# Kernel optimization log

Measured on AMD Instinct MI355X. Metric: run time of the kernel, lower is better.

The kernel has to match this reference:

```python
import jax, jax.numpy as jnp
import numpy as np

H = 8  # num_heads

def setup_inputs() -> dict:
    key = jax.random.key(0)
    ks = jax.random.split(key, 10)
    B, N, C = 2048, 50, 256
    x = jax.random.normal(ks[0], (B, N, C), dtype=jnp.float32)
    adj = jax.random.uniform(ks[1], (B, N, N), dtype=jnp.float32)
    matrix = jax.random.normal(ks[2], (B, N, N), dtype=jnp.float32)
    s = 0.02
    Wq = jax.random.normal(ks[3], (C, C), dtype=jnp.float32) * s
    bq = jnp.zeros((C,), dtype=jnp.float32)
    Wk = jax.random.normal(ks[4], (C, C), dtype=jnp.float32) * s
    bk = jnp.zeros((C,), dtype=jnp.float32)
    Wa = jax.random.normal(ks[5], (N * H, N), dtype=jnp.float32) * s
    ba = jnp.zeros((N * H,), dtype=jnp.float32)
    Wm = jax.random.normal(ks[6], (N * H, N), dtype=jnp.float32) * s
    bm = jnp.zeros((N * H,), dtype=jnp.float32)
    lambdas = jnp.tile(jnp.array([[1.0, 0.0, 0.0]], dtype=jnp.float32), (H, 1))
    return {"x": x, "adj": adj, "matrix": matrix, "Wq": Wq, "bq": bq,
            "Wk": Wk, "bk": bk, "Wa": Wa, "ba": ba, "Wm": Wm, "bm": bm,
            "lambdas": lambdas}

def reference(x, adj, matrix, Wq, bq, Wk, bk, Wa, ba, Wm, bm, lambdas):
    B, N, C = x.shape
    D = C // H
    # torch Linear: y = x @ W.T + b
    q = (jnp.einsum('bnc,dc->bnd', x, Wq) + bq).reshape(B, N, H, D).transpose(0, 2, 1, 3)
    k = (jnp.einsum('bnc,dc->bnd', x, Wk) + bk).reshape(B, N, H, D).transpose(0, 2, 1, 3)
    # NOTE: original code computes v with self.k (faithful to source)
    v = k
    # scale uses full dim C (x.shape[-1]), not head_dim, as in source
    attn = jax.nn.softmax(jnp.einsum('bhnd,bhmd->bhnm', q, k) * (C ** -0.5), axis=-1)
    adj_a = jax.nn.softmax(
        (jnp.einsum('bnm,km->bnk', adj, Wa) + ba).reshape(B, N, H, N).transpose(0, 2, 1, 3), axis=-1)
    mat_a = jax.nn.softmax(
        (jnp.einsum('bnm,km->bnk', matrix, Wm) + bm).reshape(B, N, H, N).transpose(0, 2, 1, 3), axis=-1)
    lam = jax.nn.softmax(lambdas, axis=-1)  # [H, 3]
    l0 = lam[:, 0][None, :, None, None]
    l1 = lam[:, 1][None, :, None, None]
    l2 = lam[:, 2][None, :, None, None]
    mix = l0 * attn + l1 * adj_a + l2 * mat_a  # [B, H, N, N]
    out = jnp.einsum('bhnm,bhmd->bhnd', mix, v).transpose(0, 2, 1, 3).reshape(B, N, C)
    return out
```

## Files before the change

### kernel.cpp

```cpp
#include <hip/hip_runtime.h>
#include <stdint.h>


typedef __attribute__((ext_vector_type(8))) short short8;
typedef __attribute__((ext_vector_type(4))) float f32x4;
typedef unsigned short u16;

#define L2E 1.4426950408889634f

__device__ __forceinline__ u16 f2bf(float f) {
  unsigned int u = __float_as_uint(f);
  u = (u + 0x7FFFu + ((u >> 16) & 1u)) >> 16;
  return (u16)u;
}
__device__ __forceinline__ unsigned cvt_pk_bf16(float a, float b) {
  unsigned r;
  asm("v_cvt_pk_bf16_f32 %0, %1, %2" : "=v"(r) : "v"(a), "v"(b));
  return r;
}
__device__ __forceinline__ float exp2_fast(float x) {
#if __has_builtin(__builtin_amdgcn_exp2f)
  return __builtin_amdgcn_exp2f(x);
#else
  return __expf(x * 0.6931471805599453f);
#endif
}
__device__ __forceinline__ void lds_fence() {
  asm volatile("s_waitcnt lgkmcnt(0)");
}

__global__ __launch_bounds__(256) void cast_all(
    const float* __restrict__ adj, const float* __restrict__ mat,
    const float* __restrict__ Wq, const float* __restrict__ Wk,
    const float* __restrict__ Wa, const float* __restrict__ Wm,
    const float* __restrict__ ba, const float* __restrict__ bm,
    u16* __restrict__ da, u16* __restrict__ dm, u16* __restrict__ wqk,
    u16* __restrict__ wab, u16* __restrict__ wmb,
    float* __restrict__ bap, float* __restrict__ bmp, float* __restrict__ maskv,
    u16* __restrict__ qws, u16* __restrict__ kws) {
  const int blk = blockIdx.x, tid = threadIdx.x;
  if (blk < 2048) {
    const int total8 = (102416 * 64) / 8;
    for (int i8 = blk * 256 + tid; i8 < total8; i8 += 2048 * 256) {
      int r = i8 >> 3, c = (i8 & 7) * 8;
      short8 oa = (short8){0,0,0,0,0,0,0,0};
      short8 om = (short8){0,0,0,0,0,0,0,0};
      if (r < 102400) {
        size_t base = (size_t)r * 50;
#pragma unroll
        for (int p = 0; p < 4; ++p) {
          int col = c + 2 * p;
          if (col < 50) {
            float2 va = *(const float2*)(adj + base + col);
            float2 vm = *(const float2*)(mat + base + col);
            oa[2*p] = f2bf(va.x); oa[2*p+1] = f2bf(va.y);
            om[2*p] = f2bf(vm.x); om[2*p+1] = f2bf(vm.y);
          }
        }
      }
      *(short8*)(da + (size_t)i8 * 8) = oa;
      *(short8*)(dm + (size_t)i8 * 8) = om;
    }
  } else if (blk < 2112) {
    int idx8 = (blk - 2048) * 256 + tid;
    int r = idx8 >> 5, c = (idx8 & 31) * 8;
    const float* src = (r < 256) ? (Wq + (size_t)r * 256 + c)
                                 : (Wk + (size_t)(r - 256) * 256 + c);
    float4 v0 = *(const float4*)(src);
    float4 v1 = *(const float4*)(src + 4);
    short8 o;
    o[0] = f2bf(v0.x); o[1] = f2bf(v0.y); o[2] = f2bf(v0.z); o[3] = f2bf(v0.w);
    o[4] = f2bf(v1.x); o[5] = f2bf(v1.y); o[6] = f2bf(v1.z); o[7] = f2bf(v1.w);
    *(short8*)(wqk + (size_t)idx8 * 8) = o;
  } else if (blk < 2216) {
    int idx = (blk - 2112) * 256 + tid;
    int r = idx >> 6, c = idx & 63;
    float va = 0.f, vm = 0.f;
    if (r < 400 && c < 50) { va = Wa[r * 50 + c]; vm = Wm[r * 50 + c]; }
    wab[idx] = f2bf(va); wmb[idx] = f2bf(vm);
  } else {
    short8 z = (short8){0,0,0,0,0,0,0,0};
    *(short8*)(qws + (size_t)819200 * 32 + tid * 8) = z;
    *(short8*)(kws + (size_t)819200 * 32 + tid * 8) = z;
#pragma unroll
    for (int j = 0; j < 2; ++j) {
      int idx = tid + 256 * j;
      int hh = idx >> 6, m = idx & 63;
      bap[idx] = (m < 50) ? ba[hh * 50 + m] * L2E : -1.0e30f;
      bmp[idx] = (m < 50) ? bm[hh * 50 + m] * L2E : -1.0e30f;
    }
    if (tid < 64) maskv[tid] = (tid < 50) ? 0.f : -1.0e30f;
  }
}

__global__ __launch_bounds__(256) void proj_kernel(
    const float* __restrict__ x, const u16* __restrict__ wqk,
    const float* __restrict__ bq, const float* __restrict__ bk,
    u16* __restrict__ qws, u16* __restrict__ kws) {
  __shared__ char xa[64 * 512];
  __shared__ char wb[64 * 512];
  const int tid = threadIdx.x;
  const int m0 = blockIdx.x * 64;

#pragma unroll
  for (int t = 0; t < 16; ++t) {
    int idx = tid + t * 256;
    int r = idx >> 6, c4 = idx & 63;
    float4 v = *(const float4*)(x + (size_t)(m0 + r) * 256 + c4 * 4);
    unsigned long long pk = (unsigned long long)f2bf(v.x)
                          | ((unsigned long long)f2bf(v.y) << 16)
                          | ((unsigned long long)f2bf(v.z) << 32)
                          | ((unsigned long long)f2bf(v.w) << 48);
    int byte = (r * 512 + c4 * 8) ^ ((r & 7) << 4);
    *(unsigned long long*)(xa + byte) = pk;
  }
  __syncthreads();

  const int w = tid >> 6, l = tid & 63, lo = l & 15, g = l >> 4;
  short8 a[8];
  const int ra = 16 * w + lo;
#pragma unroll
  for (int ks = 0; ks < 8; ++ks)
    a[ks] = *(const short8*)(xa + ((ra * 512 + ks * 64 + g * 16) ^ ((ra & 7) << 4)));
  size_t mb[4];
#pragma unroll
  for (int i = 0; i < 4; ++i) {
    int m = m0 + 16 * w + 4 * g + i;
    int b = m / 50;
    int n = m - 50 * b;
    mb[i] = (size_t)b * 12800 + (size_t)n * 32;
  }

  for (int nt = 0; nt < 8; ++nt) {
    __syncthreads();
#pragma unroll
    for (int t = 0; t < 8; ++t) {
      int idx = tid + t * 256;
      int r = idx >> 5, c8 = idx & 31;
      short8 v = *(const short8*)(wqk + (size_t)(nt * 64 + r) * 256 + c8 * 8);
      int byte = (r * 512 + c8 * 16) ^ ((r & 7) << 4);
      *(short8*)(wb + byte) = v;
    }
    __syncthreads();

    f32x4 acc[4];
#pragma unroll
    for (int tj = 0; tj < 4; ++tj) acc[tj] = (f32x4){0.f, 0.f, 0.f, 0.f};
#pragma unroll
    for (int ks = 0; ks < 8; ++ks) {
#pragma unroll
      for (int tj = 0; tj < 4; ++tj) {
        int rb = 16 * tj + lo;
        short8 bb = *(const short8*)(wb + ((rb * 512 + ks * 64 + g * 16) ^ ((rb & 7) << 4)));
        acc[tj] = __builtin_amdgcn_mfma_f32_16x16x32_bf16(a[ks], bb, acc[tj], 0, 0, 0);
      }
    }
    const int n0 = nt * 64;
#pragma unroll
    for (int tj = 0; tj < 4; ++tj) {
      int j = n0 + 16 * tj + lo;
      int jj = j & 255;
      float bias = (j < 256) ? bq[jj] : bk[jj];
      u16* dst = (j < 256) ? qws : kws;
      int hh = jj >> 5, d = jj & 31;
#pragma unroll
      for (int i = 0; i < 4; ++i)
        dst[mb[i] + (size_t)hh * 1600 + d] = f2bf(acc[tj][i] + bias);
    }
  }
}


__device__ __forceinline__ void sm_pv_tile(
    f32x4 (&S)[4], const f32x4 (&bml)[4], float sl2e, float lam,
    u16* pb, const short8 (&vb)[2][2], f32x4 (&Otj)[2], int buf, int lo, int g) {
  float p[4][4];
#pragma unroll
  for (int ti = 0; ti < 4; ++ti)
#pragma unroll
    for (int i = 0; i < 4; ++i)
      p[ti][i] = exp2_fast(S[ti][i] * sl2e + bml[ti][i]);
  float t0 = (p[0][0] + p[0][1]) + (p[0][2] + p[0][3]);
  float t1 = (p[1][0] + p[1][1]) + (p[1][2] + p[1][3]);
  float t2 = (p[2][0] + p[2][1]) + (p[2][2] + p[2][3]);
  float t3 = (p[3][0] + p[3][1]) + (p[3][2] + p[3][3]);
  float sum = (t0 + t1) + (t2 + t3);
  sum += __shfl_xor(sum, 16);
  sum += __shfl_xor(sum, 32);
  float r = lam * __builtin_amdgcn_rcpf(sum);
  u16* base = pb + buf * 1152 + lo * 72;
#pragma unroll
  for (int ti = 0; ti < 4; ++ti) {
    uint2 pk;
    pk.x = cvt_pk_bf16(p[ti][0] * r, p[ti][1] * r);
    pk.y = cvt_pk_bf16(p[ti][2] * r, p[ti][3] * r);
    *(uint2*)(base + 16 * ti + 4 * g) = pk;
  }
  lds_fence();
#pragma unroll
  for (int ks = 0; ks < 2; ++ks) {
    short8 pa = *(const short8*)(pb + buf * 1152 + lo * 72 + ks * 32 + g * 8);
#pragma unroll
    for (int tjv = 0; tjv < 2; ++tjv)
      Otj[tjv] = __builtin_amdgcn_mfma_f32_16x16x32_bf16(pa, vb[tjv][ks], Otj[tjv], 0, 0, 0);
  }
}

__device__ __forceinline__ void adj_phase(
    const u16* __restrict__ aBase, const u16* __restrict__ bBase,
    const float* __restrict__ bPad, float lam,
    u16* pb, const short8 (&vb)[2][2], f32x4 (&O)[2][2], int half, int lo, int g) {
  short8 af[4][2];
#pragma unroll
  for (int ti = 0; ti < 4; ++ti)
#pragma unroll
    for (int ks = 0; ks < 2; ++ks)
      af[ti][ks] = *(const short8*)(aBase + (size_t)(lo + 16 * ti) * 64 + ks * 32 + g * 8);
  short8 bf[2][2];
#pragma unroll
  for (int tjl = 0; tjl < 2; ++tjl) {
    int n = lo + 16 * (2 * half + tjl);
#pragma unroll
    for (int ks = 0; ks < 2; ++ks)
      bf[tjl][ks] = *(const short8*)(bBase + (size_t)n * 64 + ks * 32 + g * 8);
  }
  f32x4 bml[4];
#pragma unroll
  for (int ti = 0; ti < 4; ++ti)
    bml[ti] = *(const f32x4*)(bPad + 16 * ti + 4 * g);
#pragma unroll
  for (int tjl = 0; tjl < 2; ++tjl) {
    f32x4 S[4];
#pragma unroll
    for (int ti = 0; ti < 4; ++ti) S[ti] = (f32x4){0.f, 0.f, 0.f, 0.f};
#pragma unroll
    for (int ti = 0; ti < 4; ++ti)
      S[ti] = __builtin_amdgcn_mfma_f32_16x16x32_bf16(af[ti][0], bf[tjl][0], S[ti], 0, 0, 0);
#pragma unroll
    for (int ti = 0; ti < 4; ++ti)
      S[ti] = __builtin_amdgcn_mfma_f32_16x16x32_bf16(af[ti][1], bf[tjl][1], S[ti], 0, 0, 0);
    sm_pv_tile(S, bml, L2E, lam, pb, vb, O[tjl], tjl, lo, g);
  }
}

__global__ __launch_bounds__(256) void attn_kernel(
    const u16* __restrict__ qws, const u16* __restrict__ kws,
    const u16* __restrict__ adjb, const u16* __restrict__ matb,
    const u16* __restrict__ wab, const u16* __restrict__ wmb,
    const float* __restrict__ bap, const float* __restrict__ bmp,
    const float* __restrict__ maskv,
    const float* __restrict__ lambdas, float* __restrict__ out) {
  __shared__ u16 smem[4][2304];
  const int tid = threadIdx.x;
  const int w = tid >> 6, l = tid & 63, lo = l & 15, g = l >> 4;
  const int bh = blockIdx.x * 2 + (w >> 1);
  const int half = w & 1;
  const int b = bh >> 3, h = bh & 7;
  u16* sh = smem[w];

  float la = lambdas[h * 3 + 0], lb = lambdas[h * 3 + 1], lc = lambdas[h * 3 + 2];
  float lmx = fmaxf(la, fmaxf(lb, lc));
  float e0 = __expf(la - lmx), e1 = __expf(lb - lmx), e2 = __expf(lc - lmx);
  float einv = 1.f / (e0 + e1 + e2);
  float lam0 = e0 * einv, lam1 = e1 * einv, lam2 = e2 * einv;

  {
    const u16* kr = kws + (size_t)bh * 1600 + (size_t)l * 32;
#pragma unroll
    for (int ch = 0; ch < 4; ++ch) {
      short8 v = (short8){0, 0, 0, 0, 0, 0, 0, 0};
      if (l < 50) v = *(const short8*)(kr + ch * 8);
#pragma unroll
      for (int jj = 0; jj < 8; ++jj)
        sh[(ch * 8 + jj) * 72 + l] = (u16)v[jj];
    }
  }
  lds_fence();
  short8 vb[2][2];
#pragma unroll
  for (int tjv = 0; tjv < 2; ++tjv)
#pragma unroll
    for (int ks = 0; ks < 2; ++ks)
      vb[tjv][ks] = *(const short8*)(sh + (lo + 16 * tjv) * 72 + ks * 32 + g * 8);

  f32x4 O[2][2];
#pragma unroll
  for (int tjl = 0; tjl < 2; ++tjl)
#pragma unroll
    for (int tjv = 0; tjv < 2; ++tjv) O[tjl][tjv] = (f32x4){0.f, 0.f, 0.f, 0.f};

  {
    short8 af[4];
#pragma unroll
    for (int ti = 0; ti < 4; ++ti)
      af[ti] = *(const short8*)(kws + (size_t)bh * 1600 + (size_t)(lo + 16 * ti) * 32 + g * 8);
    short8 qf[2];
#pragma unroll
    for (int tjl = 0; tjl < 2; ++tjl)
      qf[tjl] = *(const short8*)(qws + (size_t)bh * 1600 +
                                 (size_t)(lo + 16 * (2 * half + tjl)) * 32 + g * 8);
    f32x4 bml[4];
#pragma unroll
    for (int ti = 0; ti < 4; ++ti)
      bml[ti] = *(const f32x4*)(maskv + 16 * ti + 4 * g);
#pragma unroll
    for (int tjl = 0; tjl < 2; ++tjl) {
      f32x4 S[4];
#pragma unroll
      for (int ti = 0; ti < 4; ++ti) S[ti] = (f32x4){0.f, 0.f, 0.f, 0.f};
#pragma unroll
      for (int ti = 0; ti < 4; ++ti)
        S[ti] = __builtin_amdgcn_mfma_f32_16x16x32_bf16(af[ti], qf[tjl], S[ti], 0, 0, 0);
      sm_pv_tile(S, bml, 0.0625f * L2E, lam0, sh, vb, O[tjl], tjl, lo, g);
    }
  }
  adj_phase(wab + (size_t)h * 3200, adjb + (size_t)b * 3200, bap + h * 64,
            lam1, sh, vb, O, half, lo, g);
  adj_phase(wmb + (size_t)h * 3200, matb + (size_t)b * 3200, bmp + h * 64,
            lam2, sh, vb, O, half, lo, g);

  float* ob = out + (size_t)b * 12800 + h * 32;
#pragma unroll
  for (int tjl = 0; tjl < 2; ++tjl) {
    int tj = 2 * half + tjl;
#pragma unroll
    for (int i = 0; i < 4; ++i) {
      int n = 16 * tj + 4 * g + i;
      if (n < 50) {
#pragma unroll
        for (int tjv = 0; tjv < 2; ++tjv)
          ob[(size_t)n * 256 + 16 * tjv + lo] = O[tjl][tjv][i];
      }
    }
  }
}

extern "C" void kernel_launch(void* const* d_in, const int* in_sizes, int n_in,
                              void* d_out, int out_size, void* d_ws, size_t ws_size,
                              hipStream_t stream) {
  const float* x       = (const float*)d_in[0];
  const float* adj     = (const float*)d_in[1];
  const float* mat     = (const float*)d_in[2];
  const float* Wq      = (const float*)d_in[3];
  const float* bq      = (const float*)d_in[4];
  const float* Wk      = (const float*)d_in[5];
  const float* bk      = (const float*)d_in[6];
  const float* Wa      = (const float*)d_in[7];
  const float* ba      = (const float*)d_in[8];
  const float* Wm      = (const float*)d_in[9];
  const float* bm      = (const float*)d_in[10];
  const float* lambdas = (const float*)d_in[11];
  float* out = (float*)d_out;

  char* ws = (char*)d_ws;
  u16* wqk    = (u16*)ws; ws += (size_t)512 * 256 * 2;
  u16* wab    = (u16*)ws; ws += (size_t)416 * 64 * 2;
  u16* wmb    = (u16*)ws; ws += (size_t)416 * 64 * 2;
  float* bap  = (float*)ws; ws += (size_t)512 * 4;
  float* bmp  = (float*)ws; ws += (size_t)512 * 4;
  float* mskv = (float*)ws; ws += (size_t)64 * 4;
  u16* adjb   = (u16*)ws; ws += (size_t)102416 * 64 * 2;
  u16* matb   = (u16*)ws; ws += (size_t)102416 * 64 * 2;
  u16* qws    = (u16*)ws; ws += (size_t)819264 * 32 * 2;
  u16* kws    = (u16*)ws; ws += (size_t)819264 * 32 * 2;

  cast_all<<<2217, 256, 0, stream>>>(adj, mat, Wq, Wk, Wa, Wm, ba, bm,
                                     adjb, matb, wqk, wab, wmb,
                                     bap, bmp, mskv, qws, kws);
  proj_kernel<<<1600, 256, 0, stream>>>(x, wqk, bq, bk, qws, kws);
  attn_kernel<<<8192, 256, 0, stream>>>(qws, kws, adjb, matb, wab, wmb,
                                        bap, bmp, mskv, lambdas, out);
}
```

Baseline: 233.6 us.

## Process two batches per wave across all query tiles to interleave independent work

Each wave now computes the full 50x50 attention for one head across two batch elements, where before a pair of waves split the query tiles of a single batch-head. The two independent streams are interleaved so the MFMA, exp and LDS round-trips of one can hide the latency of the other, and the Wa/Wm weight fragments are loaded once and reused for both batches. The explicit lgkmcnt fences are replaced by volatile LDS accesses, the grid shrinks to a quarter of its former size, and launch bounds request 2 blocks per CU. Risks are much higher register pressure from the doubled accumulators and fragments, and fewer waves available to hide latency.

Measured after the change: 234.5 us. Within noise of the previous version (+0.4%).

```diff
diff --git a/kernel.cpp b/kernel.cpp
--- a/kernel.cpp
+++ b/kernel.cpp
@@ -4,6 +4,8 @@
 
 typedef __attribute__((ext_vector_type(8))) short short8;
 typedef __attribute__((ext_vector_type(4))) float f32x4;
+typedef __attribute__((ext_vector_type(2))) unsigned u32x2;
+typedef __attribute__((ext_vector_type(4))) unsigned u32x4;
 typedef unsigned short u16;
 
 #define L2E 1.4426950408889634f
@@ -24,9 +26,6 @@
 #else
   return __expf(x * 0.6931471805599453f);
 #endif
-}
-__device__ __forceinline__ void lds_fence() {
-  asm volatile("s_waitcnt lgkmcnt(0)");
 }
 
 __global__ __launch_bounds__(256) void cast_all(
@@ -171,9 +170,9 @@
 }
 
 
-__device__ __forceinline__ void sm_pv_tile(
+__device__ __forceinline__ void sm_store(
     f32x4 (&S)[4], const f32x4 (&bml)[4], float sl2e, float lam,
-    u16* pb, const short8 (&vb)[2][2], f32x4 (&Otj)[2], int buf, int lo, int g) {
+    u16* pb, int buf, int lo, int g) {
   float p[4][4];
 #pragma unroll
   for (int ti = 0; ti < 4; ++ti)
@@ -188,75 +187,45 @@
   sum += __shfl_xor(sum, 16);
   sum += __shfl_xor(sum, 32);
   float r = lam * __builtin_amdgcn_rcpf(sum);
-  u16* base = pb + buf * 1152 + lo * 72;
 #pragma unroll
   for (int ti = 0; ti < 4; ++ti) {
-    uint2 pk;
+    u32x2 pk;
     pk.x = cvt_pk_bf16(p[ti][0] * r, p[ti][1] * r);
     pk.y = cvt_pk_bf16(p[ti][2] * r, p[ti][3] * r);
-    *(uint2*)(base + 16 * ti + 4 * g) = pk;
-  }
-  lds_fence();
+    *(volatile u32x2*)(pb + buf * 1152 + lo * 72 + 16 * ti + 4 * g) = pk;
+  }
+}
+
+__device__ __forceinline__ void pv_acc(
+    const u16* pb, int buf, const short8 (&vbS)[2][2], f32x4 (&Otj)[2],
+    int lo, int g) {
 #pragma unroll
   for (int ks = 0; ks < 2; ++ks) {
-    short8 pa = *(const short8*)(pb + buf * 1152 + lo * 72 + ks * 32 + g * 8);
+    u32x4 t = *(const volatile u32x4*)(pb + buf * 1152 + lo * 72 + ks * 32 + g * 8);
+    short8 pa = __builtin_bit_cast(short8, t);
 #pragma unroll
     for (int tjv = 0; tjv < 2; ++tjv)
-      Otj[tjv] = __builtin_amdgcn_mfma_f32_16x16x32_bf16(pa, vb[tjv][ks], Otj[tjv], 0, 0, 0);
-  }
-}
-
-__device__ __forceinline__ void adj_phase(
-    const u16* __restrict__ aBase, const u16* __restrict__ bBase,
-    const float* __restrict__ bPad, float lam,
-    u16* pb, const short8 (&vb)[2][2], f32x4 (&O)[2][2], int half, int lo, int g) {
-  short8 af[4][2];
-#pragma unroll
-  for (int ti = 0; ti < 4; ++ti)
-#pragma unroll
-    for (int ks = 0; ks < 2; ++ks)
-      af[ti][ks] = *(const short8*)(aBase + (size_t)(lo + 16 * ti) * 64 + ks * 32 + g * 8);
-  short8 bf[2][2];
-#pragma unroll
-  for (int tjl = 0; tjl < 2; ++tjl) {
-    int n = lo + 16 * (2 * half + tjl);
-#pragma unroll
-    for (int ks = 0; ks < 2; ++ks)
-      bf[tjl][ks] = *(const short8*)(bBase + (size_t)n * 64 + ks * 32 + g * 8);
-  }
-  f32x4 bml[4];
-#pragma unroll
-  for (int ti = 0; ti < 4; ++ti)
-    bml[ti] = *(const f32x4*)(bPad + 16 * ti + 4 * g);
-#pragma unroll
-  for (int tjl = 0; tjl < 2; ++tjl) {
-    f32x4 S[4];
-#pragma unroll
-    for (int ti = 0; ti < 4; ++ti) S[ti] = (f32x4){0.f, 0.f, 0.f, 0.f};
-#pragma unroll
-    for (int ti = 0; ti < 4; ++ti)
-      S[ti] = __builtin_amdgcn_mfma_f32_16x16x32_bf16(af[ti][0], bf[tjl][0], S[ti], 0, 0, 0);
-#pragma unroll
-    for (int ti = 0; ti < 4; ++ti)
-      S[ti] = __builtin_amdgcn_mfma_f32_16x16x32_bf16(af[ti][1], bf[tjl][1], S[ti], 0, 0, 0);
-    sm_pv_tile(S, bml, L2E, lam, pb, vb, O[tjl], tjl, lo, g);
-  }
-}
-
-__global__ __launch_bounds__(256) void attn_kernel(
+      Otj[tjv] = __builtin_amdgcn_mfma_f32_16x16x32_bf16(pa, vbS[tjv][ks], Otj[tjv], 0, 0, 0);
+  }
+}
+
+__global__ __launch_bounds__(256, 2) void attn_kernel(
     const u16* __restrict__ qws, const u16* __restrict__ kws,
     const u16* __restrict__ adjb, const u16* __restrict__ matb,
     const u16* __restrict__ wab, const u16* __restrict__ wmb,
     const float* __restrict__ bap, const float* __restrict__ bmp,
     const float* __restrict__ maskv,
     const float* __restrict__ lambdas, float* __restrict__ out) {
-  __shared__ u16 smem[4][2304];
+  __shared__ u16 smem[4][2][2304];
   const int tid = threadIdx.x;
   const int w = tid >> 6, l = tid & 63, lo = l & 15, g = l >> 4;
-  const int bh = blockIdx.x * 2 + (w >> 1);
-  const int half = w & 1;
-  const int b = bh >> 3, h = bh & 7;
-  u16* sh = smem[w];
+  const int wid = blockIdx.x * 4 + w;
+  const int h = wid & 7;
+  const int bp = wid >> 3;
+  const int b0 = 2 * bp, b1 = 2 * bp + 1;
+  const int bh0 = b0 * 8 + h, bh1 = b1 * 8 + h;
+  u16* pb0 = smem[w][0];
+  u16* pb1 = smem[w][1];
 
   float la = lambdas[h * 3 + 0], lb = lambdas[h * 3 + 1], lc = lambdas[h * 3 + 2];
   float lmx = fmaxf(la, fmaxf(lb, lc));
@@ -265,73 +234,132 @@
   float lam0 = e0 * einv, lam1 = e1 * einv, lam2 = e2 * einv;
 
   {
-    const u16* kr = kws + (size_t)bh * 1600 + (size_t)l * 32;
+    const u16* kr0 = kws + (size_t)bh0 * 1600 + (size_t)l * 32;
+    const u16* kr1 = kws + (size_t)bh1 * 1600 + (size_t)l * 32;
 #pragma unroll
     for (int ch = 0; ch < 4; ++ch) {
-      short8 v = (short8){0, 0, 0, 0, 0, 0, 0, 0};
-      if (l < 50) v = *(const short8*)(kr + ch * 8);
-#pragma unroll
-      for (int jj = 0; jj < 8; ++jj)
-        sh[(ch * 8 + jj) * 72 + l] = (u16)v[jj];
-    }
-  }
-  lds_fence();
-  short8 vb[2][2];
+      short8 v0 = (short8){0,0,0,0,0,0,0,0};
+      short8 v1 = (short8){0,0,0,0,0,0,0,0};
+      if (l < 50) {
+        v0 = *(const short8*)(kr0 + ch * 8);
+        v1 = *(const short8*)(kr1 + ch * 8);
+      }
+#pragma unroll
+      for (int jj = 0; jj < 8; ++jj) {
+        *(volatile u16*)(pb0 + (ch * 8 + jj) * 72 + l) = (u16)v0[jj];
+        *(volatile u16*)(pb1 + (ch * 8 + jj) * 72 + l) = (u16)v1[jj];
+      }
+    }
+  }
+  short8 vb0[2][2], vb1[2][2];
 #pragma unroll
   for (int tjv = 0; tjv < 2; ++tjv)
 #pragma unroll
-    for (int ks = 0; ks < 2; ++ks)
-      vb[tjv][ks] = *(const short8*)(sh + (lo + 16 * tjv) * 72 + ks * 32 + g * 8);
-
-  f32x4 O[2][2];
-#pragma unroll
-  for (int tjl = 0; tjl < 2; ++tjl)
-#pragma unroll
-    for (int tjv = 0; tjv < 2; ++tjv) O[tjl][tjv] = (f32x4){0.f, 0.f, 0.f, 0.f};
+    for (int ks = 0; ks < 2; ++ks) {
+      u32x4 t0 = *(const volatile u32x4*)(pb0 + (lo + 16 * tjv) * 72 + ks * 32 + g * 8);
+      u32x4 t1 = *(const volatile u32x4*)(pb1 + (lo + 16 * tjv) * 72 + ks * 32 + g * 8);
+      vb0[tjv][ks] = __builtin_bit_cast(short8, t0);
+      vb1[tjv][ks] = __builtin_bit_cast(short8, t1);
+    }
+
+  f32x4 O[2][4][2];
+#pragma unroll
+  for (int s = 0; s < 2; ++s)
+#pragma unroll
+    for (int tj = 0; tj < 4; ++tj)
+#pragma unroll
+      for (int tjv = 0; tjv < 2; ++tjv) O[s][tj][tjv] = (f32x4){0.f,0.f,0.f,0.f};
 
   {
-    short8 af[4];
-#pragma unroll
-    for (int ti = 0; ti < 4; ++ti)
-      af[ti] = *(const short8*)(kws + (size_t)bh * 1600 + (size_t)(lo + 16 * ti) * 32 + g * 8);
-    short8 qf[2];
-#pragma unroll
-    for (int tjl = 0; tjl < 2; ++tjl)
-      qf[tjl] = *(const short8*)(qws + (size_t)bh * 1600 +
-                                 (size_t)(lo + 16 * (2 * half + tjl)) * 32 + g * 8);
+    short8 af0[4], af1[4];
+#pragma unroll
+    for (int ti = 0; ti < 4; ++ti) {
+      af0[ti] = *(const short8*)(kws + (size_t)bh0 * 1600 + (size_t)(lo + 16 * ti) * 32 + g * 8);
+      af1[ti] = *(const short8*)(kws + (size_t)bh1 * 1600 + (size_t)(lo + 16 * ti) * 32 + g * 8);
+    }
     f32x4 bml[4];
 #pragma unroll
     for (int ti = 0; ti < 4; ++ti)
       bml[ti] = *(const f32x4*)(maskv + 16 * ti + 4 * g);
 #pragma unroll
-    for (int tjl = 0; tjl < 2; ++tjl) {
-      f32x4 S[4];
-#pragma unroll
-      for (int ti = 0; ti < 4; ++ti) S[ti] = (f32x4){0.f, 0.f, 0.f, 0.f};
-#pragma unroll
-      for (int ti = 0; ti < 4; ++ti)
-        S[ti] = __builtin_amdgcn_mfma_f32_16x16x32_bf16(af[ti], qf[tjl], S[ti], 0, 0, 0);
-      sm_pv_tile(S, bml, 0.0625f * L2E, lam0, sh, vb, O[tjl], tjl, lo, g);
-    }
-  }
-  adj_phase(wab + (size_t)h * 3200, adjb + (size_t)b * 3200, bap + h * 64,
-            lam1, sh, vb, O, half, lo, g);
-  adj_phase(wmb + (size_t)h * 3200, matb + (size_t)b * 3200, bmp + h * 64,
-            lam2, sh, vb, O, half, lo, g);
-
-  float* ob = out + (size_t)b * 12800 + h * 32;
-#pragma unroll
-  for (int tjl = 0; tjl < 2; ++tjl) {
-    int tj = 2 * half + tjl;
-#pragma unroll
-    for (int i = 0; i < 4; ++i) {
-      int n = 16 * tj + 4 * g + i;
-      if (n < 50) {
-#pragma unroll
-        for (int tjv = 0; tjv < 2; ++tjv)
-          ob[(size_t)n * 256 + 16 * tjv + lo] = O[tjl][tjv][i];
-      }
-    }
+    for (int tj = 0; tj < 4; ++tj) {
+      short8 qf0 = *(const short8*)(qws + (size_t)bh0 * 1600 + (size_t)(lo + 16 * tj) * 32 + g * 8);
+      short8 qf1 = *(const short8*)(qws + (size_t)bh1 * 1600 + (size_t)(lo + 16 * tj) * 32 + g * 8);
+      f32x4 S0[4], S1[4];
+#pragma unroll
+      for (int ti = 0; ti < 4; ++ti) { S0[ti] = (f32x4){0,0,0,0}; S1[ti] = (f32x4){0,0,0,0}; }
+#pragma unroll
+      for (int ti = 0; ti < 4; ++ti) {
+        S0[ti] = __builtin_amdgcn_mfma_f32_16x16x32_bf16(af0[ti], qf0, S0[ti], 0, 0, 0);
+        S1[ti] = __builtin_amdgcn_mfma_f32_16x16x32_bf16(af1[ti], qf1, S1[ti], 0, 0, 0);
+      }
+      sm_store(S0, bml, 0.0625f * L2E, lam0, pb0, tj & 1, lo, g);
+      sm_store(S1, bml, 0.0625f * L2E, lam0, pb1, tj & 1, lo, g);
+      pv_acc(pb0, tj & 1, vb0, O[0][tj], lo, g);
+      pv_acc(pb1, tj & 1, vb1, O[1][tj], lo, g);
+    }
+  }
+#pragma unroll
+  for (int ph = 0; ph < 2; ++ph) {
+    const u16* aBase = (ph == 0 ? wab : wmb) + (size_t)h * 3200;
+    const u16* bB0 = (ph == 0 ? adjb : matb) + (size_t)b0 * 3200;
+    const u16* bB1 = (ph == 0 ? adjb : matb) + (size_t)b1 * 3200;
+    const float* bPad = (ph == 0 ? bap : bmp) + h * 64;
+    float lamp = (ph == 0) ? lam1 : lam2;
+
+    short8 afw[4][2];
+#pragma unroll
+    for (int ti = 0; ti < 4; ++ti)
+#pragma unroll
+      for (int ks = 0; ks < 2; ++ks)
+        afw[ti][ks] = *(const short8*)(aBase + (size_t)(lo + 16 * ti) * 64 + ks * 32 + g * 8);
+    f32x4 bml[4];
+#pragma unroll
+    for (int ti = 0; ti < 4; ++ti)
+      bml[ti] = *(const f32x4*)(bPad + 16 * ti + 4 * g);
+
+#pragma unroll
+    for (int tj = 0; tj < 4; ++tj) {
+      short8 bf0[2], bf1[2];
+#pragma unroll
+      for (int ks = 0; ks < 2; ++ks) {
+        bf0[ks] = *(const short8*)(bB0 + (size_t)(lo + 16 * tj) * 64 + ks * 32 + g * 8);
+        bf1[ks] = *(const short8*)(bB1 + (size_t)(lo + 16 * tj) * 64 + ks * 32 + g * 8);
+      }
+      f32x4 S0[4], S1[4];
+#pragma unroll
+      for (int ti = 0; ti < 4; ++ti) { S0[ti] = (f32x4){0,0,0,0}; S1[ti] = (f32x4){0,0,0,0}; }
+#pragma unroll
+      for (int ti = 0; ti < 4; ++ti) {
+        S0[ti] = __builtin_amdgcn_mfma_f32_16x16x32_bf16(afw[ti][0], bf0[0], S0[ti], 0, 0, 0);
+        S1[ti] = __builtin_amdgcn_mfma_f32_16x16x32_bf16(afw[ti][0], bf1[0], S1[ti], 0, 0, 0);
+      }
+#pragma unroll
+      for (int ti = 0; ti < 4; ++ti) {
+        S0[ti] = __builtin_amdgcn_mfma_f32_16x16x32_bf16(afw[ti][1], bf0[1], S0[ti], 0, 0, 0);
+        S1[ti] = __builtin_amdgcn_mfma_f32_16x16x32_bf16(afw[ti][1], bf1[1], S1[ti], 0, 0, 0);
+      }
+      sm_store(S0, bml, L2E, lamp, pb0, tj & 1, lo, g);
+      sm_store(S1, bml, L2E, lamp, pb1, tj & 1, lo, g);
+      pv_acc(pb0, tj & 1, vb0, O[0][tj], lo, g);
+      pv_acc(pb1, tj & 1, vb1, O[1][tj], lo, g);
+    }
+  }
+
+#pragma unroll
+  for (int s = 0; s < 2; ++s) {
+    float* ob = out + (size_t)(s ? b1 : b0) * 12800 + h * 32;
+#pragma unroll
+    for (int tj = 0; tj < 4; ++tj)
+#pragma unroll
+      for (int i = 0; i < 4; ++i) {
+        int n = 16 * tj + 4 * g + i;
+        if (n < 50) {
+#pragma unroll
+          for (int tjv = 0; tjv < 2; ++tjv)
+            ob[(size_t)n * 256 + 16 * tjv + lo] = O[s][tj][tjv][i];
+        }
+      }
   }
 }
 
@@ -368,6 +396,6 @@
                                      adjb, matb, wqk, wab, wmb,
                                      bap, bmp, mskv, qws, kws);
   proj_kernel<<<1600, 256, 0, stream>>>(x, wqk, bq, bk, qws, kws);
-  attn_kernel<<<8192, 256, 0, stream>>>(qws, kws, adjb, matb, wab, wmb,
+  attn_kernel<<<2048, 256, 0, stream>>>(qws, kws, adjb, matb, wab, wmb,
                                         bap, bmp, mskv, lambdas, out);
 }
```

## Assign one wave per batch-head and hoist global loads ahead of compute

Applied to the files above, without the earlier changes.

Each wave now processes all four query tiles of a batch-head instead of splitting them across two waves, halving the grid. This removes redundant K transposes, K/weight fragment loads and adj/mat loads per head. Global loads for K, Q, adj and mat are issued early with scheduling barriers to overlap latency, and the explicit LDS wait is replaced with volatile LDS accesses. It raises register pressure and drops zeroing of padded K rows.

Measured after the change: 232.4 us. No clear change (-0.5%).

```diff
diff --git a/kernel.cpp b/kernel.cpp
--- a/kernel.cpp
+++ b/kernel.cpp
@@ -4,6 +4,8 @@
 
 typedef __attribute__((ext_vector_type(8))) short short8;
 typedef __attribute__((ext_vector_type(4))) float f32x4;
+typedef __attribute__((ext_vector_type(2))) unsigned u32x2;
+typedef __attribute__((ext_vector_type(4))) unsigned u32x4;
 typedef unsigned short u16;
 
 #define L2E 1.4426950408889634f
@@ -24,9 +26,6 @@
 #else
   return __expf(x * 0.6931471805599453f);
 #endif
-}
-__device__ __forceinline__ void lds_fence() {
-  asm volatile("s_waitcnt lgkmcnt(0)");
 }
 
 __global__ __launch_bounds__(256) void cast_all(
@@ -170,10 +169,9 @@
   }
 }
 
-
-__device__ __forceinline__ void sm_pv_tile(
+__device__ __forceinline__ void sm_store(
     f32x4 (&S)[4], const f32x4 (&bml)[4], float sl2e, float lam,
-    u16* pb, const short8 (&vb)[2][2], f32x4 (&Otj)[2], int buf, int lo, int g) {
+    u16* pb, int buf, int lo, int g) {
   float p[4][4];
 #pragma unroll
   for (int ti = 0; ti < 4; ++ti)
@@ -188,58 +186,25 @@
   sum += __shfl_xor(sum, 16);
   sum += __shfl_xor(sum, 32);
   float r = lam * __builtin_amdgcn_rcpf(sum);
-  u16* base = pb + buf * 1152 + lo * 72;
 #pragma unroll
   for (int ti = 0; ti < 4; ++ti) {
-    uint2 pk;
+    u32x2 pk;
     pk.x = cvt_pk_bf16(p[ti][0] * r, p[ti][1] * r);
     pk.y = cvt_pk_bf16(p[ti][2] * r, p[ti][3] * r);
-    *(uint2*)(base + 16 * ti + 4 * g) = pk;
-  }
-  lds_fence();
+    *(volatile u32x2*)(pb + buf * 1152 + lo * 72 + 16 * ti + 4 * g) = pk;
+  }
+}
+
+__device__ __forceinline__ void pv_acc(
+    const u16* pb, int buf, const short8 (&vbS)[2][2], f32x4 (&Otj)[2],
+    int lo, int g) {
 #pragma unroll
   for (int ks = 0; ks < 2; ++ks) {
-    short8 pa = *(const short8*)(pb + buf * 1152 + lo * 72 + ks * 32 + g * 8);
+    u32x4 t = *(const volatile u32x4*)(pb + buf * 1152 + lo * 72 + ks * 32 + g * 8);
+    short8 pa = __builtin_bit_cast(short8, t);
 #pragma unroll
     for (int tjv = 0; tjv < 2; ++tjv)
-      Otj[tjv] = __builtin_amdgcn_mfma_f32_16x16x32_bf16(pa, vb[tjv][ks], Otj[tjv], 0, 0, 0);
-  }
-}
-
-__device__ __forceinline__ void adj_phase(
-    const u16* __restrict__ aBase, const u16* __restrict__ bBase,
-    const float* __restrict__ bPad, float lam,
-    u16* pb, const short8 (&vb)[2][2], f32x4 (&O)[2][2], int half, int lo, int g) {
-  short8 af[4][2];
-#pragma unroll
-  for (int ti = 0; ti < 4; ++ti)
-#pragma unroll
-    for (int ks = 0; ks < 2; ++ks)
-      af[ti][ks] = *(const short8*)(aBase + (size_t)(lo + 16 * ti) * 64 + ks * 32 + g * 8);
-  short8 bf[2][2];
-#pragma unroll
-  for (int tjl = 0; tjl < 2; ++tjl) {
-    int n = lo + 16 * (2 * half + tjl);
-#pragma unroll
-    for (int ks = 0; ks < 2; ++ks)
-      bf[tjl][ks] = *(const short8*)(bBase + (size_t)n * 64 + ks * 32 + g * 8);
-  }
-  f32x4 bml[4];
-#pragma unroll
-  for (int ti = 0; ti < 4; ++ti)
-    bml[ti] = *(const f32x4*)(bPad + 16 * ti + 4 * g);
-#pragma unroll
-  for (int tjl = 0; tjl < 2; ++tjl) {
-    f32x4 S[4];
-#pragma unroll
-    for (int ti = 0; ti < 4; ++ti) S[ti] = (f32x4){0.f, 0.f, 0.f, 0.f};
-#pragma unroll
-    for (int ti = 0; ti < 4; ++ti)
-      S[ti] = __builtin_amdgcn_mfma_f32_16x16x32_bf16(af[ti][0], bf[tjl][0], S[ti], 0, 0, 0);
-#pragma unroll
-    for (int ti = 0; ti < 4; ++ti)
-      S[ti] = __builtin_amdgcn_mfma_f32_16x16x32_bf16(af[ti][1], bf[tjl][1], S[ti], 0, 0, 0);
-    sm_pv_tile(S, bml, L2E, lam, pb, vb, O[tjl], tjl, lo, g);
+      Otj[tjv] = __builtin_amdgcn_mfma_f32_16x16x32_bf16(pa, vbS[tjv][ks], Otj[tjv], 0, 0, 0);
   }
 }
 
@@ -253,10 +218,32 @@
   __shared__ u16 smem[4][2304];
   const int tid = threadIdx.x;
   const int w = tid >> 6, l = tid & 63, lo = l & 15, g = l >> 4;
-  const int bh = blockIdx.x * 2 + (w >> 1);
-  const int half = w & 1;
+  const int bh = blockIdx.x * 4 + w;
   const int b = bh >> 3, h = bh & 7;
   u16* sh = smem[w];
+
+  const u16* kbase = kws + (size_t)bh * 1600;
+  const u16* qbase = qws + (size_t)bh * 1600;
+
+  short8 kr[4];
+#pragma unroll
+  for (int ch = 0; ch < 4; ++ch)
+    kr[ch] = *(const short8*)(kbase + (size_t)l * 32 + ch * 8);
+  short8 af1[4], qf1[4];
+#pragma unroll
+  for (int ti = 0; ti < 4; ++ti)
+    af1[ti] = *(const short8*)(kbase + (size_t)(lo + 16 * ti) * 32 + g * 8);
+#pragma unroll
+  for (int tj = 0; tj < 4; ++tj)
+    qf1[tj] = *(const short8*)(qbase + (size_t)(lo + 16 * tj) * 32 + g * 8);
+  const u16* bB2 = adjb + (size_t)b * 3200;
+  short8 bf2[4][2];
+#pragma unroll
+  for (int tj = 0; tj < 4; ++tj)
+#pragma unroll
+    for (int ks = 0; ks < 2; ++ks)
+      bf2[tj][ks] = *(const short8*)(bB2 + (size_t)(lo + 16 * tj) * 64 + ks * 32 + g * 8);
+  __builtin_amdgcn_sched_barrier(0);
 
   float la = lambdas[h * 3 + 0], lb = lambdas[h * 3 + 1], lc = lambdas[h * 3 + 2];
   float lmx = fmaxf(la, fmaxf(lb, lc));
@@ -264,75 +251,120 @@
   float einv = 1.f / (e0 + e1 + e2);
   float lam0 = e0 * einv, lam1 = e1 * einv, lam2 = e2 * einv;
 
+#pragma unroll
+  for (int ch = 0; ch < 4; ++ch)
+#pragma unroll
+    for (int jj = 0; jj < 8; ++jj)
+      *(volatile u16*)(sh + (ch * 8 + jj) * 72 + l) = (u16)kr[ch][jj];
+  short8 vb[2][2];
+#pragma unroll
+  for (int tjv = 0; tjv < 2; ++tjv)
+#pragma unroll
+    for (int ks = 0; ks < 2; ++ks) {
+      u32x4 t = *(const volatile u32x4*)(sh + (lo + 16 * tjv) * 72 + ks * 32 + g * 8);
+      vb[tjv][ks] = __builtin_bit_cast(short8, t);
+    }
+
+  f32x4 O[4][2];
+#pragma unroll
+  for (int tj = 0; tj < 4; ++tj)
+#pragma unroll
+    for (int tjv = 0; tjv < 2; ++tjv) O[tj][tjv] = (f32x4){0.f, 0.f, 0.f, 0.f};
+
   {
-    const u16* kr = kws + (size_t)bh * 1600 + (size_t)l * 32;
-#pragma unroll
-    for (int ch = 0; ch < 4; ++ch) {
-      short8 v = (short8){0, 0, 0, 0, 0, 0, 0, 0};
-      if (l < 50) v = *(const short8*)(kr + ch * 8);
-#pragma unroll
-      for (int jj = 0; jj < 8; ++jj)
-        sh[(ch * 8 + jj) * 72 + l] = (u16)v[jj];
-    }
-  }
-  lds_fence();
-  short8 vb[2][2];
-#pragma unroll
-  for (int tjv = 0; tjv < 2; ++tjv)
-#pragma unroll
-    for (int ks = 0; ks < 2; ++ks)
-      vb[tjv][ks] = *(const short8*)(sh + (lo + 16 * tjv) * 72 + ks * 32 + g * 8);
-
-  f32x4 O[2][2];
-#pragma unroll
-  for (int tjl = 0; tjl < 2; ++tjl)
-#pragma unroll
-    for (int tjv = 0; tjv < 2; ++tjv) O[tjl][tjv] = (f32x4){0.f, 0.f, 0.f, 0.f};
-
-  {
-    short8 af[4];
-#pragma unroll
-    for (int ti = 0; ti < 4; ++ti)
-      af[ti] = *(const short8*)(kws + (size_t)bh * 1600 + (size_t)(lo + 16 * ti) * 32 + g * 8);
-    short8 qf[2];
-#pragma unroll
-    for (int tjl = 0; tjl < 2; ++tjl)
-      qf[tjl] = *(const short8*)(qws + (size_t)bh * 1600 +
-                                 (size_t)(lo + 16 * (2 * half + tjl)) * 32 + g * 8);
     f32x4 bml[4];
 #pragma unroll
     for (int ti = 0; ti < 4; ++ti)
       bml[ti] = *(const f32x4*)(maskv + 16 * ti + 4 * g);
 #pragma unroll
-    for (int tjl = 0; tjl < 2; ++tjl) {
+    for (int tj = 0; tj < 4; ++tj) {
       f32x4 S[4];
 #pragma unroll
       for (int ti = 0; ti < 4; ++ti) S[ti] = (f32x4){0.f, 0.f, 0.f, 0.f};
 #pragma unroll
       for (int ti = 0; ti < 4; ++ti)
-        S[ti] = __builtin_amdgcn_mfma_f32_16x16x32_bf16(af[ti], qf[tjl], S[ti], 0, 0, 0);
-      sm_pv_tile(S, bml, 0.0625f * L2E, lam0, sh, vb, O[tjl], tjl, lo, g);
-    }
-  }
-  adj_phase(wab + (size_t)h * 3200, adjb + (size_t)b * 3200, bap + h * 64,
-            lam1, sh, vb, O, half, lo, g);
-  adj_phase(wmb + (size_t)h * 3200, matb + (size_t)b * 3200, bmp + h * 64,
-            lam2, sh, vb, O, half, lo, g);
+        S[ti] = __builtin_amdgcn_mfma_f32_16x16x32_bf16(af1[ti], qf1[tj], S[ti], 0, 0, 0);
+      sm_store(S, bml, 0.0625f * L2E, lam0, sh, tj & 1, lo, g);
+      pv_acc(sh, tj & 1, vb, O[tj], lo, g);
+    }
+  }
+
+  const u16* bB3 = matb + (size_t)b * 3200;
+  short8 bf3[4][2];
+#pragma unroll
+  for (int tj = 0; tj < 4; ++tj)
+#pragma unroll
+    for (int ks = 0; ks < 2; ++ks)
+      bf3[tj][ks] = *(const short8*)(bB3 + (size_t)(lo + 16 * tj) * 64 + ks * 32 + g * 8);
+  __builtin_amdgcn_sched_barrier(0);
+
+  {
+    const u16* aBase = wab + (size_t)h * 3200;
+    short8 afw[4][2];
+#pragma unroll
+    for (int ti = 0; ti < 4; ++ti)
+#pragma unroll
+      for (int ks = 0; ks < 2; ++ks)
+        afw[ti][ks] = *(const short8*)(aBase + (size_t)(lo + 16 * ti) * 64 + ks * 32 + g * 8);
+    f32x4 bml[4];
+#pragma unroll
+    for (int ti = 0; ti < 4; ++ti)
+      bml[ti] = *(const f32x4*)(bap + h * 64 + 16 * ti + 4 * g);
+#pragma unroll
+    for (int tj = 0; tj < 4; ++tj) {
+      f32x4 S[4];
+#pragma unroll
+      for (int ti = 0; ti < 4; ++ti) S[ti] = (f32x4){0.f, 0.f, 0.f, 0.f};
+#pragma unroll
+      for (int ti = 0; ti < 4; ++ti)
+        S[ti] = __builtin_amdgcn_mfma_f32_16x16x32_bf16(afw[ti][0], bf2[tj][0], S[ti], 0, 0, 0);
+#pragma unroll
+      for (int ti = 0; ti < 4; ++ti)
+        S[ti] = __builtin_amdgcn_mfma_f32_16x16x32_bf16(afw[ti][1], bf2[tj][1], S[ti], 0, 0, 0);
+      sm_store(S, bml, L2E, lam1, sh, tj & 1, lo, g);
+      pv_acc(sh, tj & 1, vb, O[tj], lo, g);
+    }
+  }
+  {
+    const u16* aBase = wmb + (size_t)h * 3200;
+    short8 afw[4][2];
+#pragma unroll
+    for (int ti = 0; ti < 4; ++ti)
+#pragma unroll
+      for (int ks = 0; ks < 2; ++ks)
+        afw[ti][ks] = *(const short8*)(aBase + (size_t)(lo + 16 * ti) * 64 + ks * 32 + g * 8);
+    f32x4 bml[4];
+#pragma unroll
+    for (int ti = 0; ti < 4; ++ti)
+      bml[ti] = *(const f32x4*)(bmp + h * 64 + 16 * ti + 4 * g);
+#pragma unroll
+    for (int tj = 0; tj < 4; ++tj) {
+      f32x4 S[4];
+#pragma unroll
+      for (int ti = 0; ti < 4; ++ti) S[ti] = (f32x4){0.f, 0.f, 0.f, 0.f};
+#pragma unroll
+      for (int ti = 0; ti < 4; ++ti)
+        S[ti] = __builtin_amdgcn_mfma_f32_16x16x32_bf16(afw[ti][0], bf3[tj][0], S[ti], 0, 0, 0);
+#pragma unroll
+      for (int ti = 0; ti < 4; ++ti)
+        S[ti] = __builtin_amdgcn_mfma_f32_16x16x32_bf16(afw[ti][1], bf3[tj][1], S[ti], 0, 0, 0);
+      sm_store(S, bml, L2E, lam2, sh, tj & 1, lo, g);
+      pv_acc(sh, tj & 1, vb, O[tj], lo, g);
+    }
+  }
 
   float* ob = out + (size_t)b * 12800 + h * 32;
 #pragma unroll
-  for (int tjl = 0; tjl < 2; ++tjl) {
-    int tj = 2 * half + tjl;
+  for (int tj = 0; tj < 4; ++tj)
 #pragma unroll
     for (int i = 0; i < 4; ++i) {
       int n = 16 * tj + 4 * g + i;
       if (n < 50) {
 #pragma unroll
         for (int tjv = 0; tjv < 2; ++tjv)
-          ob[(size_t)n * 256 + 16 * tjv + lo] = O[tjl][tjv][i];
+          ob[(size_t)n * 256 + 16 * tjv + lo] = O[tj][tjv][i];
       }
     }
-  }
 }
 
 extern "C" void kernel_launch(void* const* d_in, const int* in_sizes, int n_in,
@@ -368,6 +400,6 @@
                                      adjb, matb, wqk, wab, wmb,
                                      bap, bmp, mskv, qws, kws);
   proj_kernel<<<1600, 256, 0, stream>>>(x, wqk, bq, bk, qws, kws);
-  attn_kernel<<<8192, 256, 0, stream>>>(qws, kws, adjb, matb, wab, wmb,
+  attn_kernel<<<4096, 256, 0, stream>>>(qws, kws, adjb, matb, wab, wmb,
                                         bap, bmp, mskv, lambdas, out);
 }
```
